# Kernel tuning notes

Measured on AMD Instinct MI355X. Metric: run time of the kernel, lower is better.

## Reference

```python
import jax, jax.numpy as jnp
import numpy as np

B, LQ, LKV = 4, 1024, 2048
QDIM, KDIM, VDIM, ODIM, H = 1024, 768, 768, 1024, 16
HD = ODIM // H  # 64


def setup_inputs() -> dict:
    key = jax.random.key(0)
    ks = jax.random.split(key, 12)
    s = 0.02
    return {
        "query": jax.random.normal(ks[0], (B, LQ, QDIM), jnp.float32),
        "key": jax.random.normal(ks[1], (B, LKV, KDIM), jnp.float32),
        "value": jax.random.normal(ks[2], (B, LKV, VDIM), jnp.float32),
        "mask": jax.random.randint(ks[3], (B, LKV), 0, 2) > 0,
        "Wq": jax.random.normal(ks[4], (QDIM, ODIM), jnp.float32) * s,
        "bq": jnp.zeros((ODIM,), jnp.float32),
        "Wk": jax.random.normal(ks[5], (KDIM, ODIM), jnp.float32) * s,
        "bk": jnp.zeros((ODIM,), jnp.float32),
        "Wv": jax.random.normal(ks[6], (VDIM, ODIM), jnp.float32) * s,
        "bv": jnp.zeros((ODIM,), jnp.float32),
        "Wo": jax.random.normal(ks[7], (ODIM, ODIM), jnp.float32) * s,
        "bo": jnp.zeros((ODIM,), jnp.float32),
    }


def reference(query, key, value, mask, Wq, bq, Wk, bk, Wv, bv, Wo, bo):
    # projections
    q = query @ Wq + bq          # [B, LQ, ODIM]
    k = key @ Wk + bk            # [B, LKV, ODIM]
    v = value @ Wv + bv          # [B, LKV, ODIM]
    # split heads -> [B, H, L, HD]
    q = q.reshape(B, LQ, H, HD).transpose(0, 2, 1, 3)
    k = k.reshape(B, LKV, H, HD).transpose(0, 2, 1, 3)
    v = v.reshape(B, LKV, H, HD).transpose(0, 2, 1, 3)
    scale = 1.0 / jnp.sqrt(jnp.asarray(HD, q.dtype))
    # scores [B, H, LQ, LKV]
    scores = jnp.einsum("bhqd,bhkd->bhqk", q, k) * scale
    # mask [B, LKV] -> broadcast over heads and query positions; True = masked
    scores = jnp.where(mask[:, None, None, :], -jnp.inf, scores)
    attn = jax.nn.softmax(scores, axis=-1)
    # dropout: eval mode (p effectively 0)
    attended = jnp.einsum("bhqk,bhkd->bhqd", attn, v)  # [B, H, LQ, HD]
    attended = attended.transpose(0, 2, 1, 3).reshape(B, LQ, ODIM)
    return attended @ Wo + bo
```

## Files before the change

kernel.cpp:

```cpp
#include <hip/hip_runtime.h>
#include <hip/hip_bf16.h>
#include <cstdint>
#include <cstddef>

using bf16 = __hip_bfloat16;
typedef __attribute__((ext_vector_type(8))) short bf16x8;
typedef __attribute__((ext_vector_type(4))) float f32x4;
typedef __attribute__((ext_vector_type(16))) float f32x16;

#define B_    4
#define LQ_   1024
#define LKV_  2048
#define QDIM_ 1024
#define KDIM_ 768
#define ODIM_ 1024
#define H_    16
#define HD_   64

__device__ __forceinline__ void async_cp16(const void* g, void* l) {
  __builtin_amdgcn_global_load_lds(
      (const __attribute__((address_space(1))) void*)g,
      (__attribute__((address_space(3))) void*)l, 16, 0, 0);
}

__device__ __forceinline__ unsigned cvtpk(float a, float b) {
  unsigned r;
  asm("v_cvt_pk_bf16_f32 %0, %1, %2" : "=v"(r) : "v"(a), "v"(b));
  return r;
}

__device__ __forceinline__ float fast_exp2(float x) {
#if __has_builtin(__builtin_amdgcn_exp2f)
  return __builtin_amdgcn_exp2f(x);
#else
  return exp2f(x);
#endif
}

__device__ __forceinline__ bf16x8 make_frag(unsigned w0, unsigned w1,
                                            unsigned w2, unsigned w3) {
  union { unsigned u[4]; bf16x8 v; } u;
  u.u[0] = w0; u.u[1] = w1; u.u[2] = w2; u.u[3] = w3;
  return u.v;
}

__global__ void mask_prep(const void* __restrict__ mraw,
                          float* __restrict__ mf, int n) {
  const int tid = threadIdx.x;
  const unsigned char* bb = (const unsigned char*)mraw;
  int local = 0;
  for (int i = tid; i < n; i += 256)
    if ((i & 3) != 0 && bb[i] != 0) local = 1;
  __shared__ int f;
  if (tid == 0) f = 0;
  __syncthreads();
  if (__any(local) && (tid & 63) == 0) atomicOr(&f, 1);
  __syncthreads();
  const int is8 = f;
  const int* w = (const int*)mraw;
  for (int i = blockIdx.x * 256 + tid; i < n; i += gridDim.x * 256)
    mf[i] = (is8 ? (int)bb[i] : (w[i] != 0)) ? 0.f : 1.f;
}

struct alignas(8) bf4 { bf16 x[4]; };

__global__ void cvt3(const float* __restrict__ q, const float* __restrict__ k,
                     const float* __restrict__ v, bf16* __restrict__ qb,
                     bf16* __restrict__ kb, bf16* __restrict__ vb) {
  const int z = blockIdx.y;
  const float* src = (z == 0) ? q : (z == 1) ? k : v;
  bf16* dst = (z == 0) ? qb : (z == 1) ? kb : vb;
  const int n4 = (z == 0) ? (B_ * LQ_ * QDIM_) / 4 : (B_ * LKV_ * KDIM_) / 4;
  const int i = blockIdx.x * 256 + threadIdx.x;
  if (i >= n4) return;
  float4 val = reinterpret_cast<const float4*>(src)[i];
  bf4 r;
  r.x[0] = __float2bfloat16(val.x);
  r.x[1] = __float2bfloat16(val.y);
  r.x[2] = __float2bfloat16(val.z);
  r.x[3] = __float2bfloat16(val.w);
  *reinterpret_cast<bf4*>(dst + (size_t)i * 4) = r;
}

__global__ void wtrans4(const float* __restrict__ Wq, const float* __restrict__ Wk,
                        const float* __restrict__ Wv, const float* __restrict__ Wo,
                        bf16* __restrict__ WqT, bf16* __restrict__ WkT,
                        bf16* __restrict__ WvT, bf16* __restrict__ WoT) {
  const int z = blockIdx.z;
  const float* W = (z == 0) ? Wq : (z == 1) ? Wk : (z == 2) ? Wv : Wo;
  bf16* WT = (z == 0) ? WqT : (z == 1) ? WkT : (z == 2) ? WvT : WoT;
  const int K = (z == 1 || z == 2) ? KDIM_ : ODIM_;
  const int N = ODIM_;
  const int n0 = blockIdx.x * 64, k0 = blockIdx.y * 64;
  if (k0 >= K) return;
  __shared__ bf16 t[64][65];
  const int tid = threadIdx.x;
#pragma unroll
  for (int i = 0; i < 16; ++i) {
    int idx = tid + i * 256;
    int nn = idx & 63, kk = idx >> 6;
    t[kk][nn] = __float2bfloat16(W[(size_t)(k0 + kk) * N + n0 + nn]);
  }
  __syncthreads();
#pragma unroll
  for (int i = 0; i < 16; ++i) {
    int idx = tid + i * 256;
    int kk = idx & 63, nn = idx >> 6;
    WT[(size_t)(n0 + nn) * K + k0 + kk] = t[kk][nn];
  }
}

__global__ void vtrans(const bf16* __restrict__ vp, bf16* __restrict__ vT) {
  __shared__ bf16 t[64][65];
  const int kv0 = blockIdx.x * 64, h = blockIdx.y, b = blockIdx.z;
  const int tid = threadIdx.x;
#pragma unroll
  for (int i = 0; i < 16; ++i) {
    int idx = tid + i * 256;
    int hd = idx & 63, kv = idx >> 6;
    t[kv][hd] = vp[(size_t)(b * LKV_ + kv0 + kv) * ODIM_ + h * HD_ + hd];
  }
  __syncthreads();
#pragma unroll
  for (int i = 0; i < 16; ++i) {
    int idx = tid + i * 256;
    int kv = idx & 63, nn = idx >> 6;
    vT[(size_t)((b * H_ + h) * HD_ + nn) * LKV_ + kv0 + kv] = t[kv][nn];
  }
}

template <int OUT_BF16>
__device__ __forceinline__ void gemm_body(const bf16* __restrict__ A,
                                          const bf16* __restrict__ BT,
                                          const float* __restrict__ bias,
                                          void* __restrict__ Cout,
                                          int M, int N, int K, int m0, int n0) {
  __shared__ bf16 As[128 * 64];
  __shared__ bf16 Bs[128 * 64];
  const int tid = threadIdx.x;
  const int lane = tid & 63, w = tid >> 6;
  const int wr = w >> 1, wc = w & 1;
  const int lr = lane & 15, lk = lane >> 4;

  f32x4 acc[4][4];
#pragma unroll
  for (int m = 0; m < 4; ++m)
#pragma unroll
    for (int n = 0; n < 4; ++n) acc[m][n] = (f32x4){0.f, 0.f, 0.f, 0.f};

  const int nk = K >> 6;
  for (int kt = 0; kt < nk; ++kt) {
    const int k0 = kt << 6;
#pragma unroll
    for (int i = 0; i < 4; ++i) {
      const int c = tid + i * 256;
      const int row = c >> 3, cc = c & 7;
      const int sc = cc ^ (row & 7);
      async_cp16(A + (size_t)(m0 + row) * K + k0 + sc * 8, As + c * 8);
    }
#pragma unroll
    for (int i = 0; i < 4; ++i) {
      const int c = tid + i * 256;
      const int row = c >> 3, cc = c & 7;
      const int sc = cc ^ (row & 7);
      async_cp16(BT + (size_t)(n0 + row) * K + k0 + sc * 8, Bs + c * 8);
    }
    asm volatile("s_waitcnt vmcnt(0)" ::: "memory");
    __syncthreads();

    bf16x8 af[4][2], bfr[4][2];
#pragma unroll
    for (int m = 0; m < 4; ++m)
#pragma unroll
      for (int ks = 0; ks < 2; ++ks) {
        const int r = wr * 64 + m * 16 + lr;
        af[m][ks] = *(const bf16x8*)((const char*)As + r * 128 +
                                     ((ks * 64 + lk * 16) ^ ((r & 7) << 4)));
      }
#pragma unroll
    for (int n = 0; n < 4; ++n)
#pragma unroll
      for (int ks = 0; ks < 2; ++ks) {
        const int r = wc * 64 + n * 16 + lr;
        bfr[n][ks] = *(const bf16x8*)((const char*)Bs + r * 128 +
                                      ((ks * 64 + lk * 16) ^ ((r & 7) << 4)));
      }
    __builtin_amdgcn_s_setprio(1);
#pragma unroll
    for (int m = 0; m < 4; ++m)
#pragma unroll
      for (int n = 0; n < 4; ++n)
#pragma unroll
        for (int ks = 0; ks < 2; ++ks)
          acc[m][n] = __builtin_amdgcn_mfma_f32_16x16x32_bf16(
              af[m][ks], bfr[n][ks], acc[m][n], 0, 0, 0);
    __builtin_amdgcn_s_setprio(0);
    __syncthreads();
  }

#pragma unroll
  for (int m = 0; m < 4; ++m)
#pragma unroll
    for (int n = 0; n < 4; ++n)
#pragma unroll
      for (int r4 = 0; r4 < 4; ++r4) {
        const int row = m0 + wr * 64 + m * 16 + lk * 4 + r4;
        const int col = n0 + wc * 64 + n * 16 + lr;
        float v = acc[m][n][r4] + bias[col];
        if (OUT_BF16)
          ((bf16*)Cout)[(size_t)row * N + col] = __float2bfloat16(v);
        else
          ((float*)Cout)[(size_t)row * N + col] = v;
      }
}

template <int OUT_BF16>
__launch_bounds__(256, 2)
__global__ void gemm_bt(const bf16* __restrict__ A, const bf16* __restrict__ BT,
                        const float* __restrict__ bias, void* __restrict__ Cout,
                        int M, int N, int K) {
  gemm_body<OUT_BF16>(A, BT, bias, Cout, M, N, K, blockIdx.y * 128,
                      blockIdx.x * 128);
}

__launch_bounds__(256, 2)
__global__ void gemm_qkv(const bf16* __restrict__ qb, const bf16* __restrict__ kb,
                         const bf16* __restrict__ vb, const bf16* __restrict__ WqT,
                         const bf16* __restrict__ WkT, const bf16* __restrict__ WvT,
                         const float* __restrict__ bq, const float* __restrict__ bk,
                         const float* __restrict__ bv, bf16* __restrict__ qp,
                         bf16* __restrict__ kp, bf16* __restrict__ vp) {
  const int z = blockIdx.z;
  const bf16* A = (z == 0) ? qb : (z == 1) ? kb : vb;
  const bf16* BT = (z == 0) ? WqT : (z == 1) ? WkT : WvT;
  const float* bias = (z == 0) ? bq : (z == 1) ? bk : bv;
  bf16* C = (z == 0) ? qp : (z == 1) ? kp : vp;
  const int M = (z == 0) ? (B_ * LQ_) : (B_ * LKV_);
  const int K = (z == 0) ? QDIM_ : KDIM_;
  const int m0 = blockIdx.y * 128;
  if (m0 >= M) return;
  gemm_body<1>(A, BT, bias, C, M, ODIM_, K, m0, blockIdx.x * 128);
}

__launch_bounds__(256, 2)
__global__ void attn5(const bf16* __restrict__ qp, const bf16* __restrict__ kp,
                      const bf16* __restrict__ vT, const float* __restrict__ mf,
                      bf16* __restrict__ att) {
  __shared__ bf16 Ks[2][64 * 64];
  __shared__ bf16 Vs[2][64 * 64];
  __shared__ float Ms[LKV_];
  const int tid = threadIdx.x;
  const int w = tid >> 6, l = tid & 63;
  const int l31 = l & 31, hi = l >> 5;
  const int d = blockIdx.x;
  const int hb = (d & 7) * 8 + ((d >> 3) & 7);
  const int qt = d >> 6;
  const int h = hb & 15, b = hb >> 4;
  const int q0 = qt * 128 + w * 32;

  const int rr = (l31 & 3) + 4 * (l31 >> 3);
  const int hh = (l31 >> 2) & 1;
  const int sig = (rr < 8) ? (8 * hh + rr) : (8 + 8 * hh + rr);

  {
    const float* msrc = mf + b * LKV_;
    async_cp16(msrc + tid * 4, &Ms[tid * 4]);
    async_cp16(msrc + 1024 + tid * 4, &Ms[1024 + tid * 4]);
  }

  bf16x8 qf[4];
  {
    const bf16* qbp =
        qp + (size_t)(b * LQ_ + q0 + l31) * ODIM_ + h * HD_ + hi * 8;
#pragma unroll
    for (int ks = 0; ks < 4; ++ks) qf[ks] = *(const bf16x8*)(qbp + ks * 16);
  }

  const int NT = LKV_ / 64;
  auto stage = [&](int t, int buf) {
    const int kv0 = (t & (NT - 1)) * 64;
#pragma unroll
    for (int i = 0; i < 2; ++i) {
      const int c = tid + i * 256;
      const int row = c >> 3, cc = c & 7, sc = cc ^ (row & 7);
      async_cp16(kp + (size_t)(b * LKV_ + kv0 + row) * ODIM_ + h * HD_ + sc * 8,
                 &Ks[buf][c * 8]);
    }
#pragma unroll
    for (int i = 0; i < 2; ++i) {
      const int c = tid + i * 256;
      const int row = c >> 3, cc = c & 7, sc = cc ^ (row & 7);
      async_cp16(vT + (size_t)((b * H_ + h) * HD_ + row) * LKV_ + kv0 + sc * 8,
                 &Vs[buf][c * 8]);
    }
  };

  f32x16 oacc0, oacc1;
#pragma unroll
  for (int r = 0; r < 16; ++r) { oacc0[r] = 0.f; oacc1[r] = 0.f; }
  float m_ = -1e30f, l_ = 0.f;
  const float csc = 0.125f * 1.4426950408889634f;

  stage(0, 0);
  for (int t = 0; t < NT; ++t) {
    const int buf = t & 1;
    stage(t + 1, buf ^ 1);
    asm volatile("s_waitcnt vmcnt(4)" ::: "memory");
    __syncthreads();

    f32x16 s0, s1;
#pragma unroll
    for (int r = 0; r < 16; ++r) { s0[r] = 0.f; s1[r] = 0.f; }
    __builtin_amdgcn_s_setprio(1);
#pragma unroll
    for (int ks = 0; ks < 4; ++ks) {
      const int ch = ks * 2 + hi;
      bf16x8 k0 = *(const bf16x8*)((const char*)&Ks[buf][0] + sig * 128 +
                                   ((ch ^ (sig & 7)) * 16));
      const int s2 = sig + 32;
      bf16x8 k1 = *(const bf16x8*)((const char*)&Ks[buf][0] + s2 * 128 +
                                   ((ch ^ (s2 & 7)) * 16));
      s0 = __builtin_amdgcn_mfma_f32_32x32x16_bf16(k0, qf[ks], s0, 0, 0, 0);
      s1 = __builtin_amdgcn_mfma_f32_32x32x16_bf16(k1, qf[ks], s1, 0, 0, 0);
    }
    __builtin_amdgcn_s_setprio(0);

    const int mb = t * 64 + hi * 8;
    f32x4 mq0[4], mq1[4];
    mq0[0] = *(const f32x4*)&Ms[mb + 0];
    mq0[1] = *(const f32x4*)&Ms[mb + 4];
    mq0[2] = *(const f32x4*)&Ms[mb + 16];
    mq0[3] = *(const f32x4*)&Ms[mb + 20];
    mq1[0] = *(const f32x4*)&Ms[mb + 32];
    mq1[1] = *(const f32x4*)&Ms[mb + 36];
    mq1[2] = *(const f32x4*)&Ms[mb + 48];
    mq1[3] = *(const f32x4*)&Ms[mb + 52];

    float rm = s0[0];
#pragma unroll
    for (int r = 1; r < 16; ++r) rm = fmaxf(rm, s0[r]);
#pragma unroll
    for (int r = 0; r < 16; ++r) rm = fmaxf(rm, s1[r]);
    rm = fmaxf(rm, __shfl_xor(rm, 32));
    const float pm = rm * csc;

    if (__any(pm > m_ + 11.0f)) {
      const float mn = fmaxf(m_, pm);
      const float alpha = fast_exp2(m_ - mn);
      l_ *= alpha;
      m_ = mn;
#pragma unroll
      for (int r = 0; r < 16; ++r) {
        const float av = __shfl(alpha, (r & 3) + 8 * (r >> 2) + 4 * hi);
        oacc0[r] *= av;
        oacc1[r] *= av;
      }
    }

    float psum = 0.f;
#pragma unroll
    for (int r = 0; r < 16; ++r) {
      float p0 = fast_exp2(fmaf(s0[r], csc, -m_)) * mq0[r >> 2][r & 3];
      float p1 = fast_exp2(fmaf(s1[r], csc, -m_)) * mq1[r >> 2][r & 3];
      s0[r] = p0;
      s1[r] = p1;
      psum += p0 + p1;
    }
    psum += __shfl_xor(psum, 32);
    l_ += psum;

    bf16x8 pa[4];
    pa[0] = make_frag(cvtpk(s0[0], s0[1]), cvtpk(s0[2], s0[3]),
                      cvtpk(s0[4], s0[5]), cvtpk(s0[6], s0[7]));
    pa[1] = make_frag(cvtpk(s0[8], s0[9]), cvtpk(s0[10], s0[11]),
                      cvtpk(s0[12], s0[13]), cvtpk(s0[14], s0[15]));
    pa[2] = make_frag(cvtpk(s1[0], s1[1]), cvtpk(s1[2], s1[3]),
                      cvtpk(s1[4], s1[5]), cvtpk(s1[6], s1[7]));
    pa[3] = make_frag(cvtpk(s1[8], s1[9]), cvtpk(s1[10], s1[11]),
                      cvtpk(s1[12], s1[13]), cvtpk(s1[14], s1[15]));

    __builtin_amdgcn_s_setprio(1);
#pragma unroll
    for (int ks = 0; ks < 4; ++ks) {
      const int ch = ks * 2 + hi;
      bf16x8 v0 = *(const bf16x8*)((const char*)&Vs[buf][0] + l31 * 128 +
                                   ((ch ^ (l31 & 7)) * 16));
      const int r2 = l31 + 32;
      bf16x8 v1 = *(const bf16x8*)((const char*)&Vs[buf][0] + r2 * 128 +
                                   ((ch ^ (r2 & 7)) * 16));
      oacc0 = __builtin_amdgcn_mfma_f32_32x32x16_bf16(pa[ks], v0, oacc0, 0, 0, 0);
      oacc1 = __builtin_amdgcn_mfma_f32_32x32x16_bf16(pa[ks], v1, oacc1, 0, 0, 0);
    }
    __builtin_amdgcn_s_setprio(0);
    __syncthreads();
  }

  const float linv = 1.0f / l_;
  const size_t obase = (size_t)(b * LQ_ + q0) * ODIM_ + h * HD_;
#pragma unroll
  for (int r = 0; r < 16; ++r) {
    const int cr = (r & 3) + 8 * (r >> 2) + 4 * hi;
    const float lv = __shfl(linv, cr);
    att[obase + (size_t)cr * ODIM_ + l31] = __float2bfloat16(oacc0[r] * lv);
    att[obase + (size_t)cr * ODIM_ + 32 + l31] = __float2bfloat16(oacc1[r] * lv);
  }
}

extern "C" void kernel_launch(void* const* d_in, const int* in_sizes, int n_in,
                              void* d_out, int out_size, void* d_ws,
                              size_t ws_size, hipStream_t stream) {
  const float* query = (const float*)d_in[0];
  const float* key   = (const float*)d_in[1];
  const float* value = (const float*)d_in[2];
  const void* mask_raw = d_in[3];
  const float* Wq = (const float*)d_in[4];
  const float* bq = (const float*)d_in[5];
  const float* Wk = (const float*)d_in[6];
  const float* bk = (const float*)d_in[7];
  const float* Wv = (const float*)d_in[8];
  const float* bv = (const float*)d_in[9];
  const float* Wo = (const float*)d_in[10];
  const float* bo = (const float*)d_in[11];
  float* out = (float*)d_out;

  char* ws = (char*)d_ws;
  bf16* qb  = (bf16*)(ws + 0);
  bf16* att = qb;
  bf16* kb  = (bf16*)(ws + 8388608);
  bf16* vb  = (bf16*)(ws + 20971520);
  bf16* vT  = (bf16*)(ws + 16777216);
  bf16* WqT = (bf16*)(ws + 33554432);
  bf16* WkT = (bf16*)(ws + 35651584);
  bf16* WvT = (bf16*)(ws + 37224448);
  bf16* WoT = (bf16*)(ws + 38797312);
  bf16* qp  = (bf16*)(ws + 40894464);
  bf16* kp  = (bf16*)(ws + 49283072);
  bf16* vp  = (bf16*)(ws + 66060288);
  float* mf = (float*)(ws + 82837504);

  mask_prep<<<32, 256, 0, stream>>>(mask_raw, mf, B_ * LKV_);

  cvt3<<<dim3(6144, 3), 256, 0, stream>>>(query, key, value, qb, kb, vb);

  wtrans4<<<dim3(16, 16, 4), 256, 0, stream>>>(Wq, Wk, Wv, Wo,
                                               WqT, WkT, WvT, WoT);

  gemm_qkv<<<dim3(8, 64, 3), 256, 0, stream>>>(qb, kb, vb, WqT, WkT, WvT,
                                               bq, bk, bv, qp, kp, vp);

  vtrans<<<dim3(32, 16, 4), 256, 0, stream>>>(vp, vT);

  attn5<<<512, 256, 0, stream>>>(qp, kp, vT, mf, att);

  gemm_bt<0><<<dim3(8, 32), 256, 0, stream>>>(att, WoT, bo, out,
                                              B_ * LQ_, ODIM_, ODIM_);
}
```

Measured before the change: 282.2 us.

## Split attention over KV halves with log-sum-exp combine kernel

Attention is split along the KV dimension into two halves, doubling the grid from 512 to 1024 blocks. Each block writes a normalized fp16 partial output plus a log-sum-exp weight, and a new combine kernel merges the two halves into bf16. The aim is better CU occupancy on a 512-block grid that underfills the GPU. It also raises the launch-bounds occupancy hints on the GEMMs and attention. This adds an extra kernel launch, workspace traffic, and fp16 rounding of the partials.

```diff
diff --git a/kernel.cpp b/kernel.cpp
--- a/kernel.cpp
+++ b/kernel.cpp
@@ -7,6 +7,7 @@
 typedef __attribute__((ext_vector_type(8))) short bf16x8;
 typedef __attribute__((ext_vector_type(4))) float f32x4;
 typedef __attribute__((ext_vector_type(16))) float f32x16;
+typedef __attribute__((ext_vector_type(8))) _Float16 f16x8;
 
 #define B_    4
 #define LQ_   1024
@@ -215,7 +216,7 @@
 }
 
 template <int OUT_BF16>
-__launch_bounds__(256, 2)
+__launch_bounds__(256, 3)
 __global__ void gemm_bt(const bf16* __restrict__ A, const bf16* __restrict__ BT,
                         const float* __restrict__ bias, void* __restrict__ Cout,
                         int M, int N, int K) {
@@ -223,7 +224,7 @@
                       blockIdx.x * 128);
 }
 
-__launch_bounds__(256, 2)
+__launch_bounds__(256, 3)
 __global__ void gemm_qkv(const bf16* __restrict__ qb, const bf16* __restrict__ kb,
                          const bf16* __restrict__ vb, const bf16* __restrict__ WqT,
                          const bf16* __restrict__ WkT, const bf16* __restrict__ WvT,
@@ -242,31 +243,29 @@
   gemm_body<1>(A, BT, bias, C, M, ODIM_, K, m0, blockIdx.x * 128);
 }
 
-__launch_bounds__(256, 2)
-__global__ void attn5(const bf16* __restrict__ qp, const bf16* __restrict__ kp,
+__launch_bounds__(256, 4)
+__global__ void attn6(const bf16* __restrict__ qp, const bf16* __restrict__ kp,
                       const bf16* __restrict__ vT, const float* __restrict__ mf,
-                      bf16* __restrict__ att) {
+                      _Float16* __restrict__ Op, float* __restrict__ Wp) {
   __shared__ bf16 Ks[2][64 * 64];
   __shared__ bf16 Vs[2][64 * 64];
-  __shared__ float Ms[LKV_];
+  __shared__ float Ms[1024];
   const int tid = threadIdx.x;
   const int w = tid >> 6, l = tid & 63;
   const int l31 = l & 31, hi = l >> 5;
   const int d = blockIdx.x;
-  const int hb = (d & 7) * 8 + ((d >> 3) & 7);
-  const int qt = d >> 6;
+  const int s = d >> 9, e = d & 511;
+  const int hb = (e & 7) * 8 + ((e >> 3) & 7);
+  const int qt = e >> 6;
   const int h = hb & 15, b = hb >> 4;
   const int q0 = qt * 128 + w * 32;
+  const int kvbase = s * 1024;
 
   const int rr = (l31 & 3) + 4 * (l31 >> 3);
   const int hh = (l31 >> 2) & 1;
   const int sig = (rr < 8) ? (8 * hh + rr) : (8 + 8 * hh + rr);
 
-  {
-    const float* msrc = mf + b * LKV_;
-    async_cp16(msrc + tid * 4, &Ms[tid * 4]);
-    async_cp16(msrc + 1024 + tid * 4, &Ms[1024 + tid * 4]);
-  }
+  async_cp16(mf + b * LKV_ + kvbase + tid * 4, &Ms[tid * 4]);
 
   bf16x8 qf[4];
   {
@@ -276,9 +275,9 @@
     for (int ks = 0; ks < 4; ++ks) qf[ks] = *(const bf16x8*)(qbp + ks * 16);
   }
 
-  const int NT = LKV_ / 64;
+  const int NT = 16;
   auto stage = [&](int t, int buf) {
-    const int kv0 = (t & (NT - 1)) * 64;
+    const int kv0 = kvbase + (t & (NT - 1)) * 64;
 #pragma unroll
     for (int i = 0; i < 2; ++i) {
       const int c = tid + i * 256;
@@ -395,14 +394,47 @@
     __syncthreads();
   }
 
-  const float linv = 1.0f / l_;
-  const size_t obase = (size_t)(b * LQ_ + q0) * ODIM_ + h * HD_;
+  const float linv = (l_ > 0.f) ? (1.0f / l_) : 0.f;
+  const float wv = (l_ > 0.f) ? (m_ + __log2f(l_)) : -1e30f;
+  if (hi == 0) Wp[((size_t)d * 4 + w) * 32 + l31] = wv;
+  _Float16* ob = Op + (size_t)d * 32768 + w * 32 * 64;
 #pragma unroll
   for (int r = 0; r < 16; ++r) {
     const int cr = (r & 3) + 8 * (r >> 2) + 4 * hi;
     const float lv = __shfl(linv, cr);
-    att[obase + (size_t)cr * ODIM_ + l31] = __float2bfloat16(oacc0[r] * lv);
-    att[obase + (size_t)cr * ODIM_ + 32 + l31] = __float2bfloat16(oacc1[r] * lv);
+    ob[cr * 64 + l31] = (_Float16)(oacc0[r] * lv);
+    ob[cr * 64 + 32 + l31] = (_Float16)(oacc1[r] * lv);
+  }
+}
+
+__global__ void attn_combine(const _Float16* __restrict__ Op,
+                             const float* __restrict__ Wp,
+                             bf16* __restrict__ att) {
+  const int e = blockIdx.x, tid = threadIdx.x;
+  const int q = tid >> 1, hd0 = (tid & 1) * 32;
+  const int hb = (e & 7) * 8 + ((e >> 3) & 7);
+  const int qt = e >> 6;
+  const int h = hb & 15, b = hb >> 4;
+  const float w0 = Wp[(size_t)e * 128 + q];
+  const float w1 = Wp[(size_t)(512 + e) * 128 + q];
+  const float mw = fmaxf(w0, w1);
+  const float c0 = fast_exp2(w0 - mw), c1 = fast_exp2(w1 - mw);
+  const float inv = 1.0f / (c0 + c1);
+  const float a0 = c0 * inv, a1 = c1 * inv;
+  const _Float16* p0 = Op + (size_t)e * 32768 + q * 64 + hd0;
+  const _Float16* p1 = p0 + (size_t)512 * 32768;
+  bf16* ob = att + (size_t)(b * LQ_ + qt * 128 + q) * ODIM_ + h * HD_ + hd0;
+#pragma unroll
+  for (int c = 0; c < 4; ++c) {
+    f16x8 v0 = *(const f16x8*)(p0 + c * 8);
+    f16x8 v1 = *(const f16x8*)(p1 + c * 8);
+    bf4 r0;
+#pragma unroll
+    for (int j = 0; j < 8; j += 2) {
+      r0.x[j & 3] = __float2bfloat16((float)v0[j] * a0 + (float)v1[j] * a1);
+      r0.x[(j + 1) & 3] = __float2bfloat16((float)v0[j + 1] * a0 + (float)v1[j + 1] * a1);
+      if ((j & 3) == 2) *reinterpret_cast<bf4*>(ob + c * 8 + (j > 3 ? 4 : 0)) = r0;
+    }
   }
 }
 
@@ -427,6 +459,7 @@
   bf16* qb  = (bf16*)(ws + 0);
   bf16* att = qb;
   bf16* kb  = (bf16*)(ws + 8388608);
+  float* Wp = (float*)(ws + 8388608);
   bf16* vb  = (bf16*)(ws + 20971520);
   bf16* vT  = (bf16*)(ws + 16777216);
   bf16* WqT = (bf16*)(ws + 33554432);
@@ -436,6 +469,7 @@
   bf16* qp  = (bf16*)(ws + 40894464);
   bf16* kp  = (bf16*)(ws + 49283072);
   bf16* vp  = (bf16*)(ws + 66060288);
+  _Float16* Op = (_Float16*)(ws + 66060288);
   float* mf = (float*)(ws + 82837504);
 
   mask_prep<<<32, 256, 0, stream>>>(mask_raw, mf, B_ * LKV_);
@@ -450,7 +484,9 @@
 
   vtrans<<<dim3(32, 16, 4), 256, 0, stream>>>(vp, vT);
 
-  attn5<<<512, 256, 0, stream>>>(qp, kp, vT, mf, att);
+  attn6<<<1024, 256, 0, stream>>>(qp, kp, vT, mf, Op, Wp);
+
+  attn_combine<<<512, 256, 0, stream>>>(Op, Wp, att);
 
   gemm_bt<0><<<dim3(8, 32), 256, 0, stream>>>(att, WoT, bo, out,
                                               B_ * LQ_, ODIM_, ODIM_);
```

After: 337.1 us. 1.19x slower.
